# Kernel optimization log

Measured on AMD Instinct MI355X. Metric: run time of the kernel, lower is better.

Reference implementation:

```python
import jax, jax.numpy as jnp
import numpy as np

EMB = 1024
HEADS = 16
FFN = 4096
EPS = 1e-5


def _layernorm(x, g, b):
    mu = jnp.mean(x, axis=-1, keepdims=True)
    var = jnp.mean((x - mu) ** 2, axis=-1, keepdims=True)
    return (x - mu) * jax.lax.rsqrt(var + EPS) * g + b


def setup_inputs() -> dict:
    key = jax.random.key(0)
    ks = jax.random.split(key, 8)
    B, T = 2, 2048
    s_in = 1.0 / np.sqrt(EMB)
    s_ffn = 1.0 / np.sqrt(FFN)
    return {
        "x": jax.random.normal(ks[0], (B, T, EMB), jnp.float32),
        "positions": jnp.arange(B * T, dtype=jnp.int64 if jax.config.jax_enable_x64 else jnp.int32).reshape(B, T),
        "ln1_g": jnp.ones((EMB,), jnp.float32),
        "ln1_b": jnp.zeros((EMB,), jnp.float32),
        "ln2_g": jnp.ones((EMB,), jnp.float32),
        "ln2_b": jnp.zeros((EMB,), jnp.float32),
        "Wq": jax.random.normal(ks[1], (EMB, EMB), jnp.float32) * s_in,
        "bq": jnp.zeros((EMB,), jnp.float32),
        "Wk": jax.random.normal(ks[2], (EMB, EMB), jnp.float32) * s_in,
        "bk": jnp.zeros((EMB,), jnp.float32),
        "Wv": jax.random.normal(ks[3], (EMB, EMB), jnp.float32) * s_in,
        "bv": jnp.zeros((EMB,), jnp.float32),
        "Wo": jax.random.normal(ks[4], (EMB, EMB), jnp.float32) * s_in,
        "bo": jnp.zeros((EMB,), jnp.float32),
        "W1": jax.random.normal(ks[5], (EMB, FFN), jnp.float32) * s_in,
        "b1": jnp.zeros((FFN,), jnp.float32),
        "W2": jax.random.normal(ks[6], (FFN, EMB), jnp.float32) * s_ffn,
        "b2": jnp.zeros((EMB,), jnp.float32),
    }


def reference(x, positions, ln1_g, ln1_b, ln2_g, ln2_b,
              Wq, bq, Wk, bk, Wv, bv, Wo, bo, W1, b1, W2, b2):
    B, T, C = x.shape
    H, D = HEADS, C // HEADS
    # x = ln1(x); then residual branches add onto the normalized x (as in source)
    x = _layernorm(x, ln1_g, ln1_b)
    # --- self attention (rope=None, mask=None, dropout inactive) ---
    q = (x @ Wq + bq).reshape(B, T, H, D).transpose(0, 2, 1, 3)  # [B,H,T,D]
    k = (x @ Wk + bk).reshape(B, T, H, D).transpose(0, 2, 1, 3)
    v = (x @ Wv + bv).reshape(B, T, H, D).transpose(0, 2, 1, 3)
    scale = 1.0 / jnp.sqrt(jnp.asarray(D, x.dtype))
    attn = jnp.einsum("bhtd,bhsd->bhts", q, k) * scale  # [B,H,T,T]
    attn = jax.nn.softmax(attn, axis=-1)
    attn_out = jnp.einsum("bhts,bhsd->bhtd", attn, v)
    attn_out = attn_out.transpose(0, 2, 1, 3).reshape(B, T, C)
    attn_out = attn_out @ Wo + bo
    x = x + attn_out
    # --- FFN with exact (erf) GELU, matching torch nn.GELU default ---
    h = _layernorm(x, ln2_g, ln2_b)
    h = jax.nn.gelu(h @ W1 + b1, approximate=False)
    h = h @ W2 + b2
    return x + h
```

## Files before the change

### kernel.cpp

```cpp
#include <hip/hip_runtime.h>
#include <cstdint>
#include <cstddef>

typedef __bf16 bf16;
typedef __bf16 bf16x8 __attribute__((ext_vector_type(8)));
typedef __bf16 bf16x4 __attribute__((ext_vector_type(4)));
typedef float f32x4 __attribute__((ext_vector_type(4)));
typedef float f32x16 __attribute__((ext_vector_type(16)));

#define TOKENS 4096
#define TSEQ   2048
#define NHEADS 16
#define HDIM   64
#define CDIM   1024

typedef __attribute__((address_space(3))) unsigned int lds_uint;
typedef __attribute__((address_space(1))) const unsigned int g_uint;
__device__ __forceinline__ void glds16(const bf16* g, bf16* l) {
  __builtin_amdgcn_global_load_lds((g_uint*)g, (lds_uint*)l, 16, 0, 0);
}

__device__ __forceinline__ float gelu_f(float v) {
  float g2 = v * (1.5957691216f + 0.0713548163f * v * v);
  return v / (1.0f + __expf(-g2));
}

#define NBUF 17
struct DetectArgs { const void* p[NBUF]; int n[NBUF]; };

__global__ __launch_bounds__(256) void detect_kernel(DetectArgs a, int* __restrict__ flags) {
  __shared__ int s_nz, s_bl;
  if (threadIdx.x == 0) { s_nz = 0; s_bl = 0; }
  __syncthreads();
  int i = blockIdx.x;
  const unsigned int* w = (const unsigned int*)a.p[i];
  int nwords = a.n[i] / 2; if (nwords > 2048) nwords = 2048;
  int nz = 0, bl = 0;
  for (int j = threadIdx.x; j < nwords; j += 256) {
    unsigned int v = w[j];
    if (v != 0u) {
      nz++;
      unsigned int e = (v >> 7) & 0xFFu;
      if (e >= 100u && e <= 140u) bl++;
    }
  }
  atomicAdd(&s_nz, nz);
  atomicAdd(&s_bl, bl);
  __syncthreads();
  if (threadIdx.x == 0) flags[i] = (2 * s_bl >= s_nz) ? 1 : 0;
}

__device__ __forceinline__ float ld_any(const void* p, size_t idx, bool isb) {
  return isb ? (float)((const bf16*)p)[idx] : ((const float*)p)[idx];
}

__device__ __forceinline__ void ln_stats(float s, float s2, int tid, float& mu, float& rstd) {
#pragma unroll
  for (int off = 32; off; off >>= 1) {
    s  += __shfl_down(s, off);
    s2 += __shfl_down(s2, off);
  }
  __shared__ float red[8];
  int w = tid >> 6;
  if ((tid & 63) == 0) { red[w] = s; red[4 + w] = s2; }
  __syncthreads();
  if (tid == 0) {
    red[0] = red[0] + red[1] + red[2] + red[3];
    red[4] = red[4] + red[5] + red[6] + red[7];
  }
  __syncthreads();
  mu = red[0] * (1.0f / CDIM);
  float var = fmaxf(red[4] * (1.0f / CDIM) - mu * mu, 0.f);
  rstd = rsqrtf(var + 1e-5f);
}

__global__ __launch_bounds__(256) void ln_f32(const float* __restrict__ x,
                                              const bf16* __restrict__ g,
                                              const bf16* __restrict__ b,
                                              bf16* __restrict__ y) {
  int row = blockIdx.x, tid = threadIdx.x;
  float v[4]; float s = 0.f, s2 = 0.f;
#pragma unroll
  for (int i = 0; i < 4; i++) {
    float f = x[(size_t)row * CDIM + tid * 4 + i];
    v[i] = f; s += f; s2 += f * f;
  }
  float mu, rstd;
  ln_stats(s, s2, tid, mu, rstd);
  bf16* yr = y + (size_t)row * CDIM;
#pragma unroll
  for (int i = 0; i < 4; i++) {
    int c = tid * 4 + i;
    yr[c] = (bf16)((v[i] - mu) * rstd * (float)g[c] + (float)b[c]);
  }
}

struct MegaArgs {
  const void* w_in[6]; bf16* w_out[6]; int wK[6], wN[6], wflag[6];
  const void* vp[10]; bf16* vd[10]; int vn[10], vfi[10];
  const void* x; const void* graw; const void* braw; bf16* y;
};

__global__ __launch_bounds__(256) void mega_pre(MegaArgs a, const int* __restrict__ flags) {
  int bid = blockIdx.x;
  int tx = threadIdx.x, ty = threadIdx.y;
  int tid = tx + ty * 64;
  if (bid < 3072) {
    __shared__ bf16 tile[64][65];
    int mi, start;
    if (bid < 1024)      { mi = bid >> 8; start = mi << 8; }
    else if (bid < 2048) { mi = 4; start = 1024; }
    else                 { mi = 5; start = 2048; }
    int tb = bid - start;
    int nT = a.wN[mi] >> 6;
    int kb = (tb / nT) * 64, nb = (tb % nT) * 64;
    int K = a.wK[mi], N = a.wN[mi];
    bool isb = flags[a.wflag[mi]] != 0;
    const void* in = a.w_in[mi]; bf16* out = a.w_out[mi];
    for (int i = ty; i < 64; i += 4)
      tile[i][tx] = (bf16)ld_any(in, (size_t)(kb + i) * N + nb + tx, isb);
    __syncthreads();
    for (int i = ty; i < 64; i += 4)
      out[(size_t)(nb + i) * K + kb + tx] = tile[tx][i];
  } else if (bid == 3072) {
    for (int i = 0; i < 10; i++) {
      bool isb = flags[a.vfi[i]] != 0;
      const void* in = a.vp[i]; bf16* out = a.vd[i]; int n = a.vn[i];
      for (int j = tid; j < n; j += 256)
        out[j] = (bf16)ld_any(in, j, isb);
    }
  } else {
    int row = bid - 3073;
    bool isb  = flags[0] != 0;
    bool gisb = flags[1] != 0;
    bool bisb = flags[2] != 0;
    float v[4]; float s = 0.f, s2 = 0.f;
#pragma unroll
    for (int i = 0; i < 4; i++) {
      float f = ld_any(a.x, (size_t)row * CDIM + tid * 4 + i, isb);
      v[i] = f; s += f; s2 += f * f;
    }
    float mu, rstd;
    ln_stats(s, s2, tid, mu, rstd);
    bf16* yr = a.y + (size_t)row * CDIM;
#pragma unroll
    for (int i = 0; i < 4; i++) {
      int c = tid * 4 + i;
      float gv = ld_any(a.graw, c, gisb);
      float bv = ld_any(a.braw, c, bisb);
      yr[c] = (bf16)((v[i] - mu) * rstd * gv + bv);
    }
  }
}

template <int BM, int BN>
__device__ __forceinline__ void gemm_core(const bf16* __restrict__ A,
                                          const bf16* __restrict__ Bt,
                                          int K, int m0, int n0,
                                          bf16* As, bf16* Bs,
                                          f32x4 (&acc)[BM / 32][BN / 32]) {
  constexpr int SI = BM / 32, SJ = BN / 32;
  int t = threadIdx.x;
  int wave = t >> 6, lane = t & 63, quad = lane >> 4, l16 = lane & 15;
  int wm = (wave & 1) * (BM / 2), wn = (wave >> 1) * (BN / 2);
  int srow = t >> 2, sc = t & 3;
  int swz = (srow >> 1) & 3;
  const bf16* ga[BM / 64];
  const bf16* gb[BN / 64];
#pragma unroll
  for (int h = 0; h < BM / 64; h++)
    ga[h] = A + (size_t)(m0 + h * 64 + srow) * K + (sc ^ swz) * 8;
#pragma unroll
  for (int h = 0; h < BN / 64; h++)
    gb[h] = Bt + (size_t)(n0 + h * 64 + srow) * K + (sc ^ swz) * 8;

  for (int k0 = 0; k0 < K; k0 += 64) {
#pragma unroll
    for (int q = 0; q < 2; q++) {
#pragma unroll
      for (int h = 0; h < BM / 64; h++)
        glds16(ga[h] + k0 + q * 32, As + q * (BM * 32) + h * 2048 + srow * 32 + sc * 8);
#pragma unroll
      for (int h = 0; h < BN / 64; h++)
        glds16(gb[h] + k0 + q * 32, Bs + q * (BN * 32) + h * 2048 + srow * 32 + sc * 8);
    }
    __syncthreads();
#pragma unroll
    for (int q = 0; q < 2; q++) {
      bf16x8 af[SI], bfr[SJ];
#pragma unroll
      for (int i = 0; i < SI; i++) {
        int m = wm + i * 16 + l16;
        af[i] = *(const bf16x8*)&As[q * (BM * 32) + m * 32 + ((quad ^ ((m >> 1) & 3)) * 8)];
      }
#pragma unroll
      for (int j = 0; j < SJ; j++) {
        int n = wn + j * 16 + l16;
        bfr[j] = *(const bf16x8*)&Bs[q * (BN * 32) + n * 32 + ((quad ^ ((n >> 1) & 3)) * 8)];
      }
#pragma unroll
      for (int i = 0; i < SI; i++)
#pragma unroll
        for (int j = 0; j < SJ; j++)
          acc[i][j] = __builtin_amdgcn_mfma_f32_16x16x32_bf16(af[i], bfr[j], acc[i][j], 0, 0, 0);
    }
    __syncthreads();
  }
}

#define EPI_NONE 0
#define EPI_RES  1
#define EPI_GELU 2

template <int BM, int BN, int EPI, typename OutT, typename ResT>
__global__ __launch_bounds__(256) void gemm128(const bf16* __restrict__ A,
                                               const bf16* __restrict__ Bt,
                                               const bf16* __restrict__ bias,
                                               const ResT* __restrict__ res,
                                               OutT* __restrict__ C,
                                               int N, int K) {
  __shared__ alignas(16) bf16 As[2 * BM * 32];
  __shared__ alignas(16) bf16 Bs[2 * BN * 32];
  int m0 = blockIdx.y * BM, n0 = blockIdx.x * BN;
  f32x4 acc[BM / 32][BN / 32] = {};
  gemm_core<BM, BN>(A, Bt, K, m0, n0, As, Bs, acc);

  int t = threadIdx.x, wave = t >> 6, lane = t & 63, quad = lane >> 4, l16 = lane & 15;
  int wm = (wave & 1) * (BM / 2), wn = (wave >> 1) * (BN / 2);
#pragma unroll
  for (int i = 0; i < BM / 32; i++)
#pragma unroll
    for (int j = 0; j < BN / 32; j++) {
      int n = n0 + wn + j * 16 + l16;
      float bv = (float)bias[n];
#pragma unroll
      for (int r = 0; r < 4; r++) {
        int m = m0 + wm + i * 16 + quad * 4 + r;
        float v = acc[i][j][r] + bv;
        if (EPI == EPI_GELU)      v = gelu_f(v);
        else if (EPI == EPI_RES)  v += (float)res[(size_t)m * N + n];
        C[(size_t)m * N + n] = (OutT)v;
      }
    }
}

__device__ __forceinline__ void gemm256_core(const bf16* __restrict__ A,
                                             const bf16* __restrict__ Bt,
                                             int K, int lda, int ldb, int m0, int n0,
                                             bf16* sm, f32x4 (&acc)[8][4]) {
  const int NT = K >> 6;
  const int t = threadIdx.x;
  const int lane = t & 63, quad = lane >> 4, l16 = lane & 15;
  const int wave = t >> 6;
  const int wm = (wave & 1) * 128, wn = (wave >> 1) * 64;
  const int srow = t >> 2, sc = t & 3;
  const int swz = (srow >> 1) & 3;
  const int rA = (srow & 63) + ((srow >> 6) << 7);
  const bf16* gA = A + (size_t)(m0 + rA) * lda + ((sc ^ swz) << 3);
  const bf16* gB = Bt + (size_t)(n0 + srow) * ldb + ((sc ^ swz) << 3);
  const int ldsA = rA * 32 + sc * 8;
  const int ldsB = srow * 32 + sc * 8;

  auto stA = [&](int tile, int u) {
    if (tile >= NT) return;
    const bf16* g = gA + (size_t)(u << 6) * lda + (tile << 6);
    bf16* l = sm + ((tile & 1) << 15) + ldsA + (u << 11);
    glds16(g, l);
    glds16(g + 32, l + 8192);
  };
  auto stB = [&](int tile, int h) {
    if (tile >= NT) return;
    const bf16* g = gB + (size_t)(h << 7) * ldb + (tile << 6);
    bf16* l = sm + ((tile & 1) << 15) + 16384 + ldsB + (h << 12);
    glds16(g, l);
    glds16(g + 32, l + 8192);
  };

  stB(0, 0); stB(0, 1); stA(0, 0); stA(0, 1);
  stB(1, 0); stB(1, 1); stA(1, 0);
  asm volatile("s_waitcnt vmcnt(6)" ::: "memory");
  __builtin_amdgcn_s_barrier();
  asm volatile("" ::: "memory");

  bf16x8 bfr[2][4];

#define LDB256(buf)                                                        \
  _Pragma("unroll") for (int q = 0; q < 2; q++)                            \
  _Pragma("unroll") for (int j = 0; j < 4; j++) {                          \
    int nl = wn + j * 16 + l16;                                            \
    bfr[q][j] = *(const bf16x8*)&sm[((buf) << 15) + 16384 + q * 8192 +     \
                                    nl * 32 + ((quad ^ ((nl >> 1) & 3)) << 3)]; \
  }

#define PHASE256(buf, P, STAGE, EXTRAWAIT)                                 \
  {                                                                        \
    bf16x8 af[2][2];                                                       \
    _Pragma("unroll") for (int q = 0; q < 2; q++)                          \
    _Pragma("unroll") for (int i2 = 0; i2 < 2; i2++) {                     \
      int ml = wm + (P) * 32 + i2 * 16 + l16;                              \
      af[q][i2] = *(const bf16x8*)&sm[((buf) << 15) + q * 8192 + ml * 32 + \
                                      ((quad ^ ((ml >> 1) & 3)) << 3)];    \
    }                                                                      \
    if ((P) == 0) { LDB256(buf); }                                         \
    STAGE;                                                                 \
    asm volatile("" ::: "memory");                                         \
    __builtin_amdgcn_s_barrier();                                          \
    asm volatile("s_waitcnt lgkmcnt(0)" ::: "memory");                     \
    __builtin_amdgcn_s_setprio(1);                                         \
    _Pragma("unroll") for (int q = 0; q < 2; q++)                          \
    _Pragma("unroll") for (int i2 = 0; i2 < 2; i2++)                       \
    _Pragma("unroll") for (int j = 0; j < 4; j++)                          \
      acc[(P) * 2 + i2][j] = __builtin_amdgcn_mfma_f32_16x16x32_bf16(      \
          af[q][i2], bfr[q][j], acc[(P) * 2 + i2][j], 0, 0, 0);            \
    __builtin_amdgcn_s_setprio(0);                                         \
    asm volatile("" ::: "memory");                                         \
    EXTRAWAIT;                                                             \
    __builtin_amdgcn_s_barrier();                                          \
    asm volatile("" ::: "memory");                                         \
  }

  for (int t0 = 0; t0 < NT; t0 += 2) {
    const int t1 = t0 + 1;
    PHASE256(0, 0, stA(t1, 1), (void)0);
    PHASE256(0, 1, stB(t0 + 2, 0), (void)0);
    PHASE256(0, 2, stB(t0 + 2, 1), (void)0);
    PHASE256(0, 3, stA(t0 + 2, 0),
             asm volatile("s_waitcnt vmcnt(6)" ::: "memory"));
    PHASE256(1, 0, stA(t0 + 2, 1), (void)0);
    PHASE256(1, 1, stB(t1 + 2, 0), (void)0);
    PHASE256(1, 2, stB(t1 + 2, 1), (void)0);
    PHASE256(1, 3, stA(t1 + 2, 0),
             asm volatile("s_waitcnt vmcnt(6)" ::: "memory"));
  }
#undef PHASE256
#undef LDB256
}

__device__ __forceinline__ void xcd_swizzle(int& bx, int& by) {
  int gx = gridDim.x;
  int nwg = gx * gridDim.y;
  int bid = blockIdx.x + blockIdx.y * gx;
  int wg = (bid & 7) * (nwg >> 3) + (bid >> 3);
  bx = wg % gx; by = wg / gx;
}

__global__ __launch_bounds__(512, 2) void gemm256_gelu(const bf16* __restrict__ A,
                                                       const bf16* __restrict__ Bt,
                                                       const bf16* __restrict__ bias,
                                                       bf16* __restrict__ C,
                                                       int N, int K) {
  __shared__ alignas(16) bf16 sm[65536];
  int bx, by; xcd_swizzle(bx, by);
  int m0 = by * 256, n0 = bx * 256;
  f32x4 acc[8][4] = {};
  gemm256_core(A, Bt, K, K, K, m0, n0, sm, acc);

  int t = threadIdx.x, wave = t >> 6, lane = t & 63, quad = lane >> 4, l16 = lane & 15;
  int wm = (wave & 1) * 128, wn = (wave >> 1) * 64;
#pragma unroll
  for (int i = 0; i < 8; i++)
#pragma unroll
    for (int j = 0; j < 4; j++) {
      int n = n0 + wn + j * 16 + l16;
      float bv = (float)bias[n];
#pragma unroll
      for (int r = 0; r < 4; r++) {
        int m = m0 + wm + i * 16 + quad * 4 + r;
        C[(size_t)m * N + n] = (bf16)gelu_f(acc[i][j][r] + bv);
      }
    }
}

__global__ __launch_bounds__(512, 2) void gemm256_part(const bf16* __restrict__ A,
                                                       const bf16* __restrict__ Bt,
                                                       bf16* __restrict__ P0, bf16* __restrict__ P1,
                                                       bf16* __restrict__ P2, bf16* __restrict__ P3,
                                                       int lda) {
  __shared__ alignas(16) bf16 sm[65536];
  int m0 = blockIdx.y * 256, n0 = blockIdx.x * 256, kz = blockIdx.z;
  const bf16* Ak = A + (size_t)kz * 1024;
  const bf16* Bk = Bt + (size_t)kz * 1024;
  f32x4 acc[8][4] = {};
  gemm256_core(Ak, Bk, 1024, lda, lda, m0, n0, sm, acc);

  bf16* P = (kz == 0) ? P0 : (kz == 1) ? P1 : (kz == 2) ? P2 : P3;
  int t = threadIdx.x, wave = t >> 6, lane = t & 63, quad = lane >> 4, l16 = lane & 15;
  int wm = (wave & 1) * 128, wn = (wave >> 1) * 64;
#pragma unroll
  for (int i = 0; i < 8; i++)
#pragma unroll
    for (int j = 0; j < 4; j++) {
      int n = n0 + wn + j * 16 + l16;
#pragma unroll
      for (int r = 0; r < 4; r++) {
        int m = m0 + wm + i * 16 + quad * 4 + r;
        P[(size_t)m * 1024 + n] = (bf16)acc[i][j][r];
      }
    }
}

__global__ __launch_bounds__(256) void w2_reduce(const bf16* __restrict__ P0, const bf16* __restrict__ P1,
                                                 const bf16* __restrict__ P2, const bf16* __restrict__ P3,
                                                 const float* __restrict__ res, const bf16* __restrict__ bias,
                                                 float* __restrict__ out) {
  int c = threadIdx.x * 4;
  size_t base = (size_t)blockIdx.x * 1024 + c;
  bf16x4 a0 = *(const bf16x4*)&P0[base];
  bf16x4 a1 = *(const bf16x4*)&P1[base];
  bf16x4 a2 = *(const bf16x4*)&P2[base];
  bf16x4 a3 = *(const bf16x4*)&P3[base];
  f32x4 rv = *(const f32x4*)&res[base];
  f32x4 o;
#pragma unroll
  for (int i = 0; i < 4; i++)
    o[i] = ((float)a0[i] + (float)a1[i]) + ((float)a2[i] + (float)a3[i]) + rv[i] + (float)bias[c + i];
  *(f32x4*)&out[base] = o;
}

__global__ __launch_bounds__(512, 2) void gemm256_qkv(const bf16* __restrict__ A,
                                                      const bf16* __restrict__ Bt,
                                                      const bf16* __restrict__ bias,
                                                      bf16* __restrict__ QK,
                                                      bf16* __restrict__ Vt) {
  __shared__ alignas(16) bf16 sm[65536];
  int bx, by; xcd_swizzle(bx, by);
  int m0 = by * 256, n0 = bx * 256;
  f32x4 acc[8][4] = {};
  gemm256_core(A, Bt, 1024, 1024, 1024, m0, n0, sm, acc);

  int t = threadIdx.x, wave = t >> 6, lane = t & 63, quad = lane >> 4, l16 = lane & 15;
  int wm = (wave & 1) * 128, wn = (wave >> 1) * 64;
#pragma unroll
  for (int i = 0; i < 8; i++)
#pragma unroll
    for (int j = 0; j < 4; j++) {
      int n = n0 + wn + j * 16 + l16;
      float bv = (float)bias[n];
      int mb = m0 + wm + i * 16 + quad * 4;
      if (n < 1024) {
#pragma unroll
        for (int r = 0; r < 4; r++)
          QK[(size_t)(mb + r) * 2048 + n] = (bf16)((acc[i][j][r] + bv) * 0.18033688011112042f);
      } else if (n < 2048) {
#pragma unroll
        for (int r = 0; r < 4; r++)
          QK[(size_t)(mb + r) * 2048 + n] = (bf16)(acc[i][j][r] + bv);
      } else {
        int qt = (mb >> 2) & 3;
        int qt2 = ((qt & 1) << 1) | (qt >> 1);
        int mb2 = (mb & ~15) | (qt2 << 2);
        bf16x4 pk;
#pragma unroll
        for (int r = 0; r < 4; r++) pk[r] = (bf16)(acc[i][j][r] + bv);
        *(bf16x4*)&Vt[(size_t)(n - 2048) * TOKENS + mb2] = pk;
      }
    }
}

__global__ __launch_bounds__(256, 2) void attn_kernel(const bf16* __restrict__ QK,
                                                      const bf16* __restrict__ Vt,
                                                      bf16* __restrict__ O) {
  __shared__ alignas(16) bf16 KV[4][8192];
  int bid = blockIdx.x;
  int xcd = bid & 7, slot = bid >> 3;
  int g = xcd + 8 * (slot >> 4);
  int q0 = (slot & 15) * 128;
  int h = g & 15, b = g >> 4;
  int t = threadIdx.x, wave = t >> 6, lane = t & 63;
  int l31 = lane & 31, l5 = lane >> 5, l7 = lane & 7;

  const bf16* Qg = QK;
  const bf16* Kg = QK + 1024;
  const size_t bT = (size_t)b * TSEQ;
  const int h64 = h * 64;

  int sr = lane >> 3;
  int sch = l7 ^ sr;
  auto stage = [&](int tile, int buf) {
    size_t krow = bT + tile * 64 + wave * 8 + sr;
    bf16* kd = &KV[buf][wave * 512 + lane * 8];
    glds16(&Kg[krow * 2048 + h64 + sch * 8], kd);
    glds16(&Kg[(krow + 32) * 2048 + h64 + sch * 8], kd + 2048);
    size_t vrow = (size_t)(h64 + wave * 8 + sr) * TOKENS + bT + tile * 64 + sch * 8;
    glds16(&Vt[vrow], kd + 4096);
    glds16(&Vt[vrow + (size_t)32 * TOKENS], kd + 6144);
  };

  bf16x8 qf[4];
  {
    size_t qrow = bT + q0 + wave * 32 + l31;
    const bf16* qp = &Qg[qrow * 2048 + h64 + l5 * 8];
#pragma unroll
    for (int ds = 0; ds < 4; ds++) qf[ds] = *(const bf16x8*)(qp + ds * 16);
  }

  int off[4];
#pragma unroll
  for (int w = 0; w < 4; w++) off[w] = l31 * 64 + (((w * 2 + l5) ^ l7) * 8);

  f32x16 accO0 = {}, accO1 = {}, accL = {};
  const bf16 one = (bf16)1.0f;
  const bf16x8 onesv = {one, one, one, one, one, one, one, one};

  stage(0, 0);
  stage(1, 1);
  asm volatile("s_waitcnt vmcnt(4)" ::: "memory");
  __builtin_amdgcn_s_barrier();
  asm volatile("" ::: "memory");

  for (int it4 = 0; it4 < TSEQ / 64; it4 += 4) {
#pragma unroll
    for (int u = 0; u < 4; u++) {
      int it = it4 + u;
      if (it + 2 < TSEQ / 64) stage(it + 2, (it + 2) & 3);
      const bf16* KB = &KV[u][0];

      f32x16 st0 = {}, st1 = {};
      __builtin_amdgcn_s_setprio(1);
#pragma unroll
      for (int ds = 0; ds < 4; ds++) {
        bf16x8 k0 = *(const bf16x8*)&KB[off[ds]];
        bf16x8 k1 = *(const bf16x8*)&KB[off[ds] + 2048];
        st0 = __builtin_amdgcn_mfma_f32_32x32x16_bf16(k0, qf[ds], st0, 0, 0, 0);
        st1 = __builtin_amdgcn_mfma_f32_32x32x16_bf16(k1, qf[ds], st1, 0, 0, 0);
      }
      __builtin_amdgcn_s_setprio(0);

      bf16x8 pa[4];
#pragma unroll
      for (int j = 0; j < 8; j++) {
        pa[0][j] = (bf16)exp2f(fminf(st0[j], 86.f));
        pa[1][j] = (bf16)exp2f(fminf(st0[8 + j], 86.f));
        pa[2][j] = (bf16)exp2f(fminf(st1[j], 86.f));
        pa[3][j] = (bf16)exp2f(fminf(st1[8 + j], 86.f));
      }

      __builtin_amdgcn_s_setprio(1);
#pragma unroll
      for (int w = 0; w < 4; w++) {
        bf16x8 v0 = *(const bf16x8*)&KB[off[w] + 4096];
        bf16x8 v1 = *(const bf16x8*)&KB[off[w] + 6144];
        accO0 = __builtin_amdgcn_mfma_f32_32x32x16_bf16(pa[w], v0, accO0, 0, 0, 0);
        accO1 = __builtin_amdgcn_mfma_f32_32x32x16_bf16(pa[w], v1, accO1, 0, 0, 0);
        accL  = __builtin_amdgcn_mfma_f32_32x32x16_bf16(pa[w], onesv, accL, 0, 0, 0);
      }
      __builtin_amdgcn_s_setprio(0);

      if (it + 2 < TSEQ / 64)
        asm volatile("s_waitcnt vmcnt(4)" ::: "memory");
      else
        asm volatile("s_waitcnt vmcnt(0)" ::: "memory");
      __builtin_amdgcn_s_barrier();
      asm volatile("" ::: "memory");
    }
  }

#pragma unroll
  for (int r = 0; r < 16; r++) {
    int q = (r & 3) + 8 * (r >> 2) + 4 * l5;
    float rl = 1.0f / fmaxf(accL[r], 1e-30f);
    size_t orow = (bT + q0 + wave * 32 + q) * CDIM + h64;
    O[orow + l31]      = (bf16)(accO0[r] * rl);
    O[orow + 32 + l31] = (bf16)(accO1[r] * rl);
  }
}

extern "C" void kernel_launch(void* const* d_in, const int* in_sizes, int n_in,
                              void* d_out, int out_size, void* d_ws, size_t ws_size,
                              hipStream_t stream) {
  char* ws = (char*)d_ws;
  const size_t MB = 1024 * 1024;
  const size_t KB = 1024;

  int* flags = (int*)ws;
  bf16* vec_c = (bf16*)(ws + 4 * KB);
  bf16* ln1g_c = vec_c + 0 * 8192;
  bf16* ln1b_c = vec_c + 1 * 8192;
  bf16* ln2g_c = vec_c + 2 * 8192;
  bf16* ln2b_c = vec_c + 3 * 8192;
  bf16* bqkv_c = vec_c + 4 * 8192;
  bf16* bo_c   = vec_c + 6 * 8192;
  bf16* b1_c   = vec_c + 7 * 8192;
  bf16* b2_c   = vec_c + 8 * 8192;

  bf16*  WqkvT  = (bf16*)(ws + 1 * MB);
  bf16*  WoT    = (bf16*)(ws + 7 * MB);
  bf16*  W1T    = (bf16*)(ws + 9 * MB);
  bf16*  W2T    = (bf16*)(ws + 17 * MB);
  bf16*  xn     = (bf16*)(ws + 25 * MB);
  bf16*  QKbuf  = (bf16*)(ws + 33 * MB);
  bf16*  Vtbuf  = (bf16*)(ws + 49 * MB);
  bf16*  ab     = (bf16*)(ws + 57 * MB);
  float* xmid32 = (float*)(ws + 65 * MB);
  bf16*  h2     = (bf16*)(ws + 81 * MB);
  bf16*  f1     = (bf16*)(ws + 33 * MB);
  bf16*  pk0    = (bf16*)(ws + 49 * MB);
  bf16*  pk1    = (bf16*)(ws + 57 * MB);
  bf16*  pk2    = (bf16*)(ws + 1 * MB);
  bf16*  pk3    = (bf16*)(ws + 9 * MB);

  const int din_idx[NBUF] = {0, 2, 3, 4, 5, 6, 7, 8, 9, 10, 11, 12, 13, 14, 15, 16, 17};
  DetectArgs da;
  for (int i = 0; i < NBUF; i++) { da.p[i] = d_in[din_idx[i]]; da.n[i] = in_sizes[din_idx[i]]; }
  detect_kernel<<<NBUF, 256, 0, stream>>>(da, flags);

  MegaArgs ma;
  {
    const void* wi[6] = {d_in[6], d_in[8], d_in[10], d_in[12], d_in[14], d_in[16]};
    bf16* wo[6] = {WqkvT, WqkvT + 1024 * 1024, WqkvT + 2 * 1024 * 1024, WoT, W1T, W2T};
    const int wK[6] = {1024, 1024, 1024, 1024, 1024, 4096};
    const int wN[6] = {1024, 1024, 1024, 1024, 4096, 1024};
    const int wf[6] = {5, 7, 9, 11, 13, 15};
    for (int i = 0; i < 6; i++) {
      ma.w_in[i] = wi[i]; ma.w_out[i] = wo[i];
      ma.wK[i] = wK[i]; ma.wN[i] = wN[i]; ma.wflag[i] = wf[i];
    }
    const int vf[10] = {1, 2, 3, 4, 6, 8, 10, 12, 14, 16};
    bf16* vd[10] = {ln1g_c, ln1b_c, ln2g_c, ln2b_c,
                    bqkv_c, bqkv_c + 1024, bqkv_c + 2048, bo_c, b1_c, b2_c};
    for (int i = 0; i < 10; i++) {
      int di = din_idx[vf[i]];
      ma.vp[i] = d_in[di]; ma.vd[i] = vd[i]; ma.vn[i] = in_sizes[di]; ma.vfi[i] = vf[i];
    }
    ma.x = d_in[0]; ma.graw = d_in[2]; ma.braw = d_in[3]; ma.y = xn;
  }
  mega_pre<<<3072 + 1 + TOKENS, dim3(64, 4), 0, stream>>>(ma, flags);

  gemm256_qkv<<<dim3(12, 16), 512, 0, stream>>>(xn, WqkvT, bqkv_c, QKbuf, Vtbuf);

  attn_kernel<<<512, 256, 0, stream>>>(QKbuf, Vtbuf, ab);

  gemm128<64, 128, EPI_RES, float, bf16><<<dim3(8, 64), 256, 0, stream>>>(
      ab, WoT, bo_c, xn, xmid32, 1024, 1024);

  ln_f32<<<TOKENS, 256, 0, stream>>>(xmid32, ln2g_c, ln2b_c, h2);

  gemm256_gelu<<<dim3(16, 16), 512, 0, stream>>>(h2, W1T, b1_c, f1, 4096, 1024);

  gemm256_part<<<dim3(4, 16, 4), 512, 0, stream>>>(f1, W2T, pk0, pk1, pk2, pk3, 4096);
  w2_reduce<<<TOKENS, 256, 0, stream>>>(pk0, pk1, pk2, pk3, xmid32, b2_c, (float*)d_out);
}
```

Before: 364.7 us.

## Split attention key range across two wave groups and reduce through LDS

The attention kernel now runs 512 threads per block. Two groups of four waves each process half of the key/value tiles, using double-buffered LDS staging per group instead of a single four-deep ring. At the end, the second group writes its partial O and row-sum accumulators to LDS, and the first group adds them before normalising and storing. This raises the number of waves per CU to hide latency in the exp and MFMA loop, at the cost of an extra LDS reduction and more barrier synchronisation. Two W2 partial-sum buffers are also moved to other workspace regions.

```diff
diff --git a/kernel.cpp b/kernel.cpp
--- a/kernel.cpp
+++ b/kernel.cpp
@@ -457,38 +457,41 @@
     }
 }
 
-__global__ __launch_bounds__(256, 2) void attn_kernel(const bf16* __restrict__ QK,
+__global__ __launch_bounds__(512, 2) void attn_kernel(const bf16* __restrict__ QK,
                                                       const bf16* __restrict__ Vt,
                                                       bf16* __restrict__ O) {
-  __shared__ alignas(16) bf16 KV[4][8192];
+  __shared__ alignas(16) bf16 KV[2][2][8192];
   int bid = blockIdx.x;
   int xcd = bid & 7, slot = bid >> 3;
   int g = xcd + 8 * (slot >> 4);
   int q0 = (slot & 15) * 128;
   int h = g & 15, b = g >> 4;
   int t = threadIdx.x, wave = t >> 6, lane = t & 63;
+  int ws4 = wave & 3, str = wave >> 2;
   int l31 = lane & 31, l5 = lane >> 5, l7 = lane & 7;
 
   const bf16* Qg = QK;
   const bf16* Kg = QK + 1024;
   const size_t bT = (size_t)b * TSEQ;
   const int h64 = h * 64;
+  const int tb0 = str * 16;
 
   int sr = lane >> 3;
   int sch = l7 ^ sr;
   auto stage = [&](int tile, int buf) {
-    size_t krow = bT + tile * 64 + wave * 8 + sr;
-    bf16* kd = &KV[buf][wave * 512 + lane * 8];
+    int gt = tb0 + tile;
+    size_t krow = bT + gt * 64 + ws4 * 8 + sr;
+    bf16* kd = &KV[str][buf][ws4 * 512 + lane * 8];
     glds16(&Kg[krow * 2048 + h64 + sch * 8], kd);
     glds16(&Kg[(krow + 32) * 2048 + h64 + sch * 8], kd + 2048);
-    size_t vrow = (size_t)(h64 + wave * 8 + sr) * TOKENS + bT + tile * 64 + sch * 8;
+    size_t vrow = (size_t)(h64 + ws4 * 8 + sr) * TOKENS + bT + gt * 64 + sch * 8;
     glds16(&Vt[vrow], kd + 4096);
     glds16(&Vt[vrow + (size_t)32 * TOKENS], kd + 6144);
   };
 
   bf16x8 qf[4];
   {
-    size_t qrow = bT + q0 + wave * 32 + l31;
+    size_t qrow = bT + q0 + ws4 * 32 + l31;
     const bf16* qp = &Qg[qrow * 2048 + h64 + l5 * 8];
 #pragma unroll
     for (int ds = 0; ds < 4; ds++) qf[ds] = *(const bf16x8*)(qp + ds * 16);
@@ -503,65 +506,68 @@
   const bf16x8 onesv = {one, one, one, one, one, one, one, one};
 
   stage(0, 0);
-  stage(1, 1);
-  asm volatile("s_waitcnt vmcnt(4)" ::: "memory");
-  __builtin_amdgcn_s_barrier();
-  asm volatile("" ::: "memory");
-
-  for (int it4 = 0; it4 < TSEQ / 64; it4 += 4) {
-#pragma unroll
-    for (int u = 0; u < 4; u++) {
-      int it = it4 + u;
-      if (it + 2 < TSEQ / 64) stage(it + 2, (it + 2) & 3);
-      const bf16* KB = &KV[u][0];
-
-      f32x16 st0 = {}, st1 = {};
-      __builtin_amdgcn_s_setprio(1);
-#pragma unroll
-      for (int ds = 0; ds < 4; ds++) {
-        bf16x8 k0 = *(const bf16x8*)&KB[off[ds]];
-        bf16x8 k1 = *(const bf16x8*)&KB[off[ds] + 2048];
-        st0 = __builtin_amdgcn_mfma_f32_32x32x16_bf16(k0, qf[ds], st0, 0, 0, 0);
-        st1 = __builtin_amdgcn_mfma_f32_32x32x16_bf16(k1, qf[ds], st1, 0, 0, 0);
-      }
-      __builtin_amdgcn_s_setprio(0);
-
-      bf16x8 pa[4];
-#pragma unroll
-      for (int j = 0; j < 8; j++) {
-        pa[0][j] = (bf16)exp2f(fminf(st0[j], 86.f));
-        pa[1][j] = (bf16)exp2f(fminf(st0[8 + j], 86.f));
-        pa[2][j] = (bf16)exp2f(fminf(st1[j], 86.f));
-        pa[3][j] = (bf16)exp2f(fminf(st1[8 + j], 86.f));
-      }
-
-      __builtin_amdgcn_s_setprio(1);
-#pragma unroll
-      for (int w = 0; w < 4; w++) {
-        bf16x8 v0 = *(const bf16x8*)&KB[off[w] + 4096];
-        bf16x8 v1 = *(const bf16x8*)&KB[off[w] + 6144];
-        accO0 = __builtin_amdgcn_mfma_f32_32x32x16_bf16(pa[w], v0, accO0, 0, 0, 0);
-        accO1 = __builtin_amdgcn_mfma_f32_32x32x16_bf16(pa[w], v1, accO1, 0, 0, 0);
-        accL  = __builtin_amdgcn_mfma_f32_32x32x16_bf16(pa[w], onesv, accL, 0, 0, 0);
-      }
-      __builtin_amdgcn_s_setprio(0);
-
-      if (it + 2 < TSEQ / 64)
-        asm volatile("s_waitcnt vmcnt(4)" ::: "memory");
-      else
-        asm volatile("s_waitcnt vmcnt(0)" ::: "memory");
-      __builtin_amdgcn_s_barrier();
-      asm volatile("" ::: "memory");
-    }
-  }
-
-#pragma unroll
-  for (int r = 0; r < 16; r++) {
-    int q = (r & 3) + 8 * (r >> 2) + 4 * l5;
-    float rl = 1.0f / fmaxf(accL[r], 1e-30f);
-    size_t orow = (bT + q0 + wave * 32 + q) * CDIM + h64;
-    O[orow + l31]      = (bf16)(accO0[r] * rl);
-    O[orow + 32 + l31] = (bf16)(accO1[r] * rl);
+  __syncthreads();
+
+  for (int it = 0; it < 16; it++) {
+    int cur = it & 1;
+    if (it + 1 < 16) stage(it + 1, cur ^ 1);
+    const bf16* KB = &KV[str][cur][0];
+
+    f32x16 st0 = {}, st1 = {};
+    __builtin_amdgcn_s_setprio(1);
+#pragma unroll
+    for (int ds = 0; ds < 4; ds++) {
+      bf16x8 k0 = *(const bf16x8*)&KB[off[ds]];
+      bf16x8 k1 = *(const bf16x8*)&KB[off[ds] + 2048];
+      st0 = __builtin_amdgcn_mfma_f32_32x32x16_bf16(k0, qf[ds], st0, 0, 0, 0);
+      st1 = __builtin_amdgcn_mfma_f32_32x32x16_bf16(k1, qf[ds], st1, 0, 0, 0);
+    }
+    __builtin_amdgcn_s_setprio(0);
+
+    bf16x8 pa[4];
+#pragma unroll
+    for (int j = 0; j < 8; j++) {
+      pa[0][j] = (bf16)exp2f(fminf(st0[j], 86.f));
+      pa[1][j] = (bf16)exp2f(fminf(st0[8 + j], 86.f));
+      pa[2][j] = (bf16)exp2f(fminf(st1[j], 86.f));
+      pa[3][j] = (bf16)exp2f(fminf(st1[8 + j], 86.f));
+    }
+
+    __builtin_amdgcn_s_setprio(1);
+#pragma unroll
+    for (int w = 0; w < 4; w++) {
+      bf16x8 v0 = *(const bf16x8*)&KB[off[w] + 4096];
+      bf16x8 v1 = *(const bf16x8*)&KB[off[w] + 6144];
+      accO0 = __builtin_amdgcn_mfma_f32_32x32x16_bf16(pa[w], v0, accO0, 0, 0, 0);
+      accO1 = __builtin_amdgcn_mfma_f32_32x32x16_bf16(pa[w], v1, accO1, 0, 0, 0);
+      accL  = __builtin_amdgcn_mfma_f32_32x32x16_bf16(pa[w], onesv, accL, 0, 0, 0);
+    }
+    __builtin_amdgcn_s_setprio(0);
+
+    __syncthreads();
+  }
+
+  float* cb = (float*)&KV[0][0][0];
+  if (str == 1) {
+    int base = ws4 * 3072 + lane * 16;
+    *(f32x16*)&cb[base]        = accO0;
+    *(f32x16*)&cb[base + 1024] = accO1;
+    *(f32x16*)&cb[base + 2048] = accL;
+  }
+  __syncthreads();
+  if (str == 0) {
+    int base = ws4 * 3072 + lane * 16;
+    f32x16 o0 = *(const f32x16*)&cb[base];
+    f32x16 o1 = *(const f32x16*)&cb[base + 1024];
+    f32x16 ll = *(const f32x16*)&cb[base + 2048];
+#pragma unroll
+    for (int r = 0; r < 16; r++) {
+      int q = (r & 3) + 8 * (r >> 2) + 4 * l5;
+      float rl = 1.0f / fmaxf(accL[r] + ll[r], 1e-30f);
+      size_t orow = (bT + q0 + ws4 * 32 + q) * CDIM + h64;
+      O[orow + l31]      = (bf16)((accO0[r] + o0[r]) * rl);
+      O[orow + 32 + l31] = (bf16)((accO1[r] + o1[r]) * rl);
+    }
   }
 }
 
@@ -594,8 +600,8 @@
   float* xmid32 = (float*)(ws + 65 * MB);
   bf16*  h2     = (bf16*)(ws + 81 * MB);
   bf16*  f1     = (bf16*)(ws + 33 * MB);
-  bf16*  pk0    = (bf16*)(ws + 49 * MB);
-  bf16*  pk1    = (bf16*)(ws + 57 * MB);
+  bf16*  pk0    = (bf16*)(ws + 25 * MB);
+  bf16*  pk1    = (bf16*)(ws + 81 * MB);
   bf16*  pk2    = (bf16*)(ws + 1 * MB);
   bf16*  pk3    = (bf16*)(ws + 9 * MB);
 
@@ -628,7 +634,7 @@
 
   gemm256_qkv<<<dim3(12, 16), 512, 0, stream>>>(xn, WqkvT, bqkv_c, QKbuf, Vtbuf);
 
-  attn_kernel<<<512, 256, 0, stream>>>(QKbuf, Vtbuf, ab);
+  attn_kernel<<<512, 512, 0, stream>>>(QKbuf, Vtbuf, ab);
 
   gemm128<64, 128, EPI_RES, float, bf16><<<dim3(8, 64), 256, 0, stream>>>(
       ab, WoT, bo_c, xn, xmid32, 1024, 1024);
```

After: 372.6 us. 1.02x slower.

## Software-pipeline attention QK and PV across iterations, vectorize LN and weight transpose

Applied to the files above, without the earlier changes.

The attention inner loop now computes the QK^T scores for tile it while doing the exp and PV MFMAs for tile it-1, using ping-pong score registers. The aim is to overlap exp/VALU work with matrix-core work. The layernorm kernels and the weight-transpose prep now use 4-wide vector loads and stores, and the transpose tile padding changes to fit them. Two packed-buffer workspace offsets are moved. The attention change holds two score tiles live at once, which raises register pressure.

```diff
diff --git a/kernel.cpp b/kernel.cpp
--- a/kernel.cpp
+++ b/kernel.cpp
@@ -79,20 +79,18 @@
                                               const bf16* __restrict__ b,
                                               bf16* __restrict__ y) {
   int row = blockIdx.x, tid = threadIdx.x;
-  float v[4]; float s = 0.f, s2 = 0.f;
-#pragma unroll
-  for (int i = 0; i < 4; i++) {
-    float f = x[(size_t)row * CDIM + tid * 4 + i];
-    v[i] = f; s += f; s2 += f * f;
-  }
+  f32x4 v = *(const f32x4*)&x[(size_t)row * CDIM + tid * 4];
+  float s = v[0] + v[1] + v[2] + v[3];
+  float s2 = v[0] * v[0] + v[1] * v[1] + v[2] * v[2] + v[3] * v[3];
   float mu, rstd;
   ln_stats(s, s2, tid, mu, rstd);
-  bf16* yr = y + (size_t)row * CDIM;
-#pragma unroll
-  for (int i = 0; i < 4; i++) {
-    int c = tid * 4 + i;
-    yr[c] = (bf16)((v[i] - mu) * rstd * (float)g[c] + (float)b[c]);
-  }
+  bf16x4 gv = *(const bf16x4*)&g[tid * 4];
+  bf16x4 bv = *(const bf16x4*)&b[tid * 4];
+  bf16x4 o;
+#pragma unroll
+  for (int i = 0; i < 4; i++)
+    o[i] = (bf16)((v[i] - mu) * rstd * (float)gv[i] + (float)bv[i]);
+  *(bf16x4*)&y[(size_t)row * CDIM + tid * 4] = o;
 }
 
 struct MegaArgs {
@@ -106,7 +104,7 @@
   int tx = threadIdx.x, ty = threadIdx.y;
   int tid = tx + ty * 64;
   if (bid < 3072) {
-    __shared__ bf16 tile[64][65];
+    __shared__ bf16 tile[64][68];
     int mi, start;
     if (bid < 1024)      { mi = bid >> 8; start = mi << 8; }
     else if (bid < 2048) { mi = 4; start = 1024; }
@@ -117,11 +115,30 @@
     int K = a.wK[mi], N = a.wN[mi];
     bool isb = flags[a.wflag[mi]] != 0;
     const void* in = a.w_in[mi]; bf16* out = a.w_out[mi];
-    for (int i = ty; i < 64; i += 4)
-      tile[i][tx] = (bf16)ld_any(in, (size_t)(kb + i) * N + nb + tx, isb);
+    int r0 = tid >> 4, c4 = (tid & 15) * 4;
+#pragma unroll
+    for (int p = 0; p < 4; p++) {
+      int r = r0 + p * 16;
+      size_t gi = (size_t)(kb + r) * N + nb + c4;
+      bf16x4 pk;
+      if (isb) {
+        pk = *(const bf16x4*)&((const bf16*)in)[gi];
+      } else {
+        f32x4 f = *(const f32x4*)&((const float*)in)[gi];
+#pragma unroll
+        for (int j = 0; j < 4; j++) pk[j] = (bf16)f[j];
+      }
+      *(bf16x4*)&tile[r][c4] = pk;
+    }
     __syncthreads();
-    for (int i = ty; i < 64; i += 4)
-      out[(size_t)(nb + i) * K + kb + tx] = tile[tx][i];
+#pragma unroll
+    for (int p = 0; p < 4; p++) {
+      int nr = r0 + p * 16;
+      bf16x4 o;
+#pragma unroll
+      for (int j = 0; j < 4; j++) o[j] = tile[c4 + j][nr];
+      *(bf16x4*)&out[(size_t)(nb + nr) * K + kb + c4] = o;
+    }
   } else if (bid == 3072) {
     for (int i = 0; i < 10; i++) {
       bool isb = flags[a.vfi[i]] != 0;
@@ -135,21 +152,27 @@
     bool gisb = flags[1] != 0;
     bool bisb = flags[2] != 0;
     float v[4]; float s = 0.f, s2 = 0.f;
-#pragma unroll
-    for (int i = 0; i < 4; i++) {
-      float f = ld_any(a.x, (size_t)row * CDIM + tid * 4 + i, isb);
-      v[i] = f; s += f; s2 += f * f;
+    size_t xi = (size_t)row * CDIM + tid * 4;
+    if (isb) {
+      bf16x4 x4 = *(const bf16x4*)&((const bf16*)a.x)[xi];
+#pragma unroll
+      for (int i = 0; i < 4; i++) { v[i] = (float)x4[i]; s += v[i]; s2 += v[i] * v[i]; }
+    } else {
+      f32x4 x4 = *(const f32x4*)&((const float*)a.x)[xi];
+#pragma unroll
+      for (int i = 0; i < 4; i++) { v[i] = x4[i]; s += v[i]; s2 += v[i] * v[i]; }
     }
     float mu, rstd;
     ln_stats(s, s2, tid, mu, rstd);
-    bf16* yr = a.y + (size_t)row * CDIM;
+    bf16x4 o;
 #pragma unroll
     for (int i = 0; i < 4; i++) {
       int c = tid * 4 + i;
       float gv = ld_any(a.graw, c, gisb);
       float bv = ld_any(a.braw, c, bisb);
-      yr[c] = (bf16)((v[i] - mu) * rstd * gv + bv);
-    }
+      o[i] = (bf16)((v[i] - mu) * rstd * gv + bv);
+    }
+    *(bf16x4*)&a.y[(size_t)row * CDIM + tid * 4] = o;
   }
 }
 
@@ -502,58 +525,73 @@
   const bf16 one = (bf16)1.0f;
   const bf16x8 onesv = {one, one, one, one, one, one, one, one};
 
+  f32x16 sA0, sA1, sB0, sB1;
+
   stage(0, 0);
   stage(1, 1);
   asm volatile("s_waitcnt vmcnt(4)" ::: "memory");
   __builtin_amdgcn_s_barrier();
   asm volatile("" ::: "memory");
 
-  for (int it4 = 0; it4 < TSEQ / 64; it4 += 4) {
-#pragma unroll
-    for (int u = 0; u < 4; u++) {
-      int it = it4 + u;
-      if (it + 2 < TSEQ / 64) stage(it + 2, (it + 2) & 3);
-      const bf16* KB = &KV[u][0];
-
-      f32x16 st0 = {}, st1 = {};
-      __builtin_amdgcn_s_setprio(1);
-#pragma unroll
-      for (int ds = 0; ds < 4; ds++) {
-        bf16x8 k0 = *(const bf16x8*)&KB[off[ds]];
-        bf16x8 k1 = *(const bf16x8*)&KB[off[ds] + 2048];
-        st0 = __builtin_amdgcn_mfma_f32_32x32x16_bf16(k0, qf[ds], st0, 0, 0, 0);
-        st1 = __builtin_amdgcn_mfma_f32_32x32x16_bf16(k1, qf[ds], st1, 0, 0, 0);
-      }
-      __builtin_amdgcn_s_setprio(0);
-
-      bf16x8 pa[4];
-#pragma unroll
-      for (int j = 0; j < 8; j++) {
-        pa[0][j] = (bf16)exp2f(fminf(st0[j], 86.f));
-        pa[1][j] = (bf16)exp2f(fminf(st0[8 + j], 86.f));
-        pa[2][j] = (bf16)exp2f(fminf(st1[j], 86.f));
-        pa[3][j] = (bf16)exp2f(fminf(st1[8 + j], 86.f));
-      }
-
-      __builtin_amdgcn_s_setprio(1);
-#pragma unroll
-      for (int w = 0; w < 4; w++) {
-        bf16x8 v0 = *(const bf16x8*)&KB[off[w] + 4096];
-        bf16x8 v1 = *(const bf16x8*)&KB[off[w] + 6144];
-        accO0 = __builtin_amdgcn_mfma_f32_32x32x16_bf16(pa[w], v0, accO0, 0, 0, 0);
-        accO1 = __builtin_amdgcn_mfma_f32_32x32x16_bf16(pa[w], v1, accO1, 0, 0, 0);
-        accL  = __builtin_amdgcn_mfma_f32_32x32x16_bf16(pa[w], onesv, accL, 0, 0, 0);
-      }
-      __builtin_amdgcn_s_setprio(0);
-
-      if (it + 2 < TSEQ / 64)
-        asm volatile("s_waitcnt vmcnt(4)" ::: "memory");
-      else
-        asm volatile("s_waitcnt vmcnt(0)" ::: "memory");
-      __builtin_amdgcn_s_barrier();
-      asm volatile("" ::: "memory");
-    }
-  }
+#define QKSTEP(S0, S1, IT)                                                  \
+  {                                                                         \
+    const bf16* KB = &KV[(IT) & 3][0];                                      \
+    S0 = (f32x16){}; S1 = (f32x16){};                                       \
+    __builtin_amdgcn_s_setprio(1);                                          \
+    _Pragma("unroll") for (int ds = 0; ds < 4; ds++) {                      \
+      bf16x8 k0 = *(const bf16x8*)&KB[off[ds]];                             \
+      bf16x8 k1 = *(const bf16x8*)&KB[off[ds] + 2048];                      \
+      S0 = __builtin_amdgcn_mfma_f32_32x32x16_bf16(k0, qf[ds], S0, 0, 0, 0);\
+      S1 = __builtin_amdgcn_mfma_f32_32x32x16_bf16(k1, qf[ds], S1, 0, 0, 0);\
+    }                                                                       \
+    __builtin_amdgcn_s_setprio(0);                                          \
+  }
+
+#define PVSTEP(P0, P1, IT)                                                  \
+  {                                                                         \
+    bf16x8 pa[4];                                                           \
+    _Pragma("unroll") for (int j = 0; j < 8; j++) {                         \
+      pa[0][j] = (bf16)exp2f(fminf(P0[j], 86.f));                           \
+      pa[1][j] = (bf16)exp2f(fminf(P0[8 + j], 86.f));                       \
+      pa[2][j] = (bf16)exp2f(fminf(P1[j], 86.f));                           \
+      pa[3][j] = (bf16)exp2f(fminf(P1[8 + j], 86.f));                       \
+    }                                                                       \
+    const bf16* VB = &KV[(IT) & 3][4096];                                   \
+    __builtin_amdgcn_s_setprio(1);                                          \
+    _Pragma("unroll") for (int w = 0; w < 4; w++) {                         \
+      bf16x8 v0 = *(const bf16x8*)&VB[off[w]];                              \
+      bf16x8 v1 = *(const bf16x8*)&VB[off[w] + 2048];                       \
+      accO0 = __builtin_amdgcn_mfma_f32_32x32x16_bf16(pa[w], v0, accO0, 0, 0, 0); \
+      accO1 = __builtin_amdgcn_mfma_f32_32x32x16_bf16(pa[w], v1, accO1, 0, 0, 0); \
+      accL  = __builtin_amdgcn_mfma_f32_32x32x16_bf16(pa[w], onesv, accL, 0, 0, 0); \
+    }                                                                       \
+    __builtin_amdgcn_s_setprio(0);                                          \
+  }
+
+#define ITER(CUR0, CUR1, PRV0, PRV1, IT, DOPV)                              \
+  {                                                                         \
+    if ((IT) + 2 < TSEQ / 64) stage((IT) + 2, ((IT) + 2) & 3);              \
+    QKSTEP(CUR0, CUR1, IT);                                                 \
+    if (DOPV) PVSTEP(PRV0, PRV1, (IT) - 1);                                 \
+    if ((IT) + 2 < TSEQ / 64)                                               \
+      asm volatile("s_waitcnt vmcnt(4)" ::: "memory");                      \
+    else                                                                    \
+      asm volatile("s_waitcnt vmcnt(0)" ::: "memory");                      \
+    __builtin_amdgcn_s_barrier();                                           \
+    asm volatile("" ::: "memory");                                          \
+  }
+
+  ITER(sA0, sA1, sB0, sB1, 0, false);
+  ITER(sB0, sB1, sA0, sA1, 1, true);
+  for (int it = 2; it < TSEQ / 64; it += 2) {
+    ITER(sA0, sA1, sB0, sB1, it, true);
+    ITER(sB0, sB1, sA0, sA1, it + 1, true);
+  }
+  PVSTEP(sB0, sB1, TSEQ / 64 - 1);
+
+#undef ITER
+#undef PVSTEP
+#undef QKSTEP
 
 #pragma unroll
   for (int r = 0; r < 16; r++) {
@@ -594,8 +632,8 @@
   float* xmid32 = (float*)(ws + 65 * MB);
   bf16*  h2     = (bf16*)(ws + 81 * MB);
   bf16*  f1     = (bf16*)(ws + 33 * MB);
-  bf16*  pk0    = (bf16*)(ws + 49 * MB);
-  bf16*  pk1    = (bf16*)(ws + 57 * MB);
+  bf16*  pk0    = (bf16*)(ws + 25 * MB);
+  bf16*  pk1    = (bf16*)(ws + 81 * MB);
   bf16*  pk2    = (bf16*)(ws + 1 * MB);
   bf16*  pk3    = (bf16*)(ws + 9 * MB);
 
```

Result: no change. 363.9 us (-0.2%).
